# Kernel optimization log

Hardware: AMD Instinct MI355X
Metric: run time of the kernel (lower is better)

## Reference

```python
import jax, jax.numpy as jnp
import numpy as np

# PEPS grid configuration (matches init_kwargs)
X, Y = 4, 4            # xnodes, ynodes
D = 6                  # bond_dim
P = 2                  # features_in (physical dim)
F = 10                 # features_out (forced by result.view([10]))
CX, CY = X // 2, Y // 2  # center node carries the output leg
BATCH = 2048


def node_labels(i, j):
    # bond labels after the physical index is contracted away; axis order: up, left, down, right, out
    labs = []
    if i > 0: labs.append(f'v{i-1}_{j}')   # up bond (shared with row i-1)
    if j > 0: labs.append(f'h{i}_{j-1}')   # left bond (shared with col j-1)
    if i < X - 1: labs.append(f'v{i}_{j}') # down bond
    if j < Y - 1: labs.append(f'h{i}_{j}') # right bond
    if (i, j) == (CX, CY): labs.append('o')  # output leg on center node
    return labs


def node_shape(i, j):
    shp = [P]  # physical axis first (input_nodes[i][j][0] ^ peps_nodes[i][j][0])
    shp += [D] * (int(i > 0) + int(j > 0) + int(i < X - 1) + int(j < Y - 1))
    if (i, j) == (CX, CY): shp.append(F)
    return tuple(shp)


def setup_inputs() -> dict:
    key = jax.random.key(0)
    keys = jax.random.split(key, X * Y + 1)
    inp = {"x": jax.random.normal(keys[0], (BATCH, X, Y, P), dtype=jnp.float32)}
    k = 1
    for i in range(X):
        for j in range(Y):
            # simple_peps uniform init with std=0.01
            inp[f"w{i}{j}"] = jax.random.uniform(keys[k], node_shape(i, j), dtype=jnp.float32, minval=-0.01, maxval=0.01)
            k += 1
    return inp


def _td(a, alabs, b, blabs):
    """Label-tracked tensordot over all shared bond labels."""
    shared = [l for l in alabs if l in blabs]
    ai = [alabs.index(l) for l in shared]
    bi = [blabs.index(l) for l in shared]
    out = jnp.tensordot(a, b, axes=(ai, bi))
    labs = [l for l in alabs if l not in shared] + [l for l in blabs if l not in shared]
    return out, labs


def _contract_sample(xs, ws):
    # xs: [X, Y, P] one sample; ws: list-of-lists of node tensors
    # 1) contract each input vector into its PEPS node over the physical axis,
    #    then L2-normalize each contracted node (as in func())
    nodes = []
    for i in range(X):
        row = []
        for j in range(Y):
            t = jnp.tensordot(xs[i, j], ws[i][j], axes=(0, 0))
            t = t / jnp.linalg.norm(t)
            row.append(t)
        nodes.append(row)
    # 2) exact contraction of the 2D network, row-by-row boundary sweep
    cur, labs = nodes[0][0], node_labels(0, 0)
    for j in range(1, Y):
        cur, labs = _td(cur, labs, nodes[0][j], node_labels(0, j))
    for i in range(1, X):
        for j in range(Y):
            cur, labs = _td(cur, labs, nodes[i][j], node_labels(i, j))
    out = cur.reshape(F)  # result.view([10])
    return out / jnp.linalg.norm(out)


def reference(x, w00, w01, w02, w03, w10, w11, w12, w13,
              w20, w21, w22, w23, w30, w31, w32, w33):
    ws = [[w00, w01, w02, w03],
          [w10, w11, w12, w13],
          [w20, w21, w22, w23],
          [w30, w31, w32, w33]]
    return jax.vmap(lambda s: _contract_sample(s, ws))(x)  # [B, F]
```

## Files before the change

### kernel.cpp

```cpp
#include <hip/hip_runtime.h>
#include <math.h>

#define NT 128
#define NS 64

struct PW { const float* w[16]; int perp[16]; };

#define TLT 64
#define TRT 20800
#define BLT 41536
#define RTT 62272

template<int X1, int X2, int Y1, int Y2, int U, int L,
         int AX1, int AX2, int AU, int AL,
         int BU, int BLs, int BY1, int BY2,
         int OX1, int OX2, int OY1, int OY2>
__device__ __forceinline__ void contract(const float* __restrict__ A,
                                         const float* __restrict__ Bm,
                                         float* __restrict__ O, int tid) {
    constexpr int ROWS = X1 * X2 * Y1;
    for (int r = tid; r < ROWS; r += NT) {
        const int x1 = r / (X2 * Y1);
        const int rm = r - x1 * (X2 * Y1);
        const int x2 = rm / Y1;
        const int y1 = rm - x2 * Y1;
        const float* __restrict__ Ab = A + x1 * AX1 + x2 * AX2;
        const float* __restrict__ Bb = Bm + y1 * BY1;
        float acc[Y2];
#pragma unroll
        for (int t = 0; t < Y2; t++) acc[t] = 0.f;
#pragma unroll
        for (int u = 0; u < U; u++) {
#pragma unroll
            for (int l = 0; l < L; l++) {
                const float a = Ab[u * AU + l * AL];
                const float* __restrict__ Bp = Bb + u * BU + l * BLs;
#pragma unroll
                for (int t = 0; t < Y2; t++) acc[t] += a * Bp[t * BY2];
            }
        }
        float* __restrict__ Ob = O + x1 * OX1 + x2 * OX2 + y1 * OY1;
#pragma unroll
        for (int t = 0; t < Y2; t++) Ob[t * OY2] = acc[t];
    }
}

template<int M, int DST>
__device__ __forceinline__ void csel(float* __restrict__ L, const float* __restrict__ W, int tid) {
    for (int e = tid; e < M; e += NT) L[DST + e] = W[e];
}

__global__ __launch_bounds__(NT) void prep(PW pw, float* __restrict__ ws) {
    __shared__ float L[4356];
    constexpr int bA = 0, bB = 1296, bC = 2592, sA = 3888, sB = 4104, sC = 4320;
    const int tid = threadIdx.x, bid = blockIdx.x;
    if (bid < 16) {
        const int p = bid;
        csel<36, sC>(L, pw.w[0] + ((p >> 0) & 1) * 36, tid);
        csel<216, sA>(L, pw.w[1] + ((p >> 1) & 1) * 216, tid);
        __syncthreads();
        contract<1,6,6,6,6,1,  0,6,1,0,  36,0,6,1,  0,36,6,1>(L+sC, L+sA, L+sB, tid);
        csel<216, bA>(L, pw.w[4] + ((p >> 2) & 1) * 216, tid);
        __syncthreads();
        contract<1,36,6,6,6,1,  0,1,36,0,  36,0,6,1,  0,36,6,1>(L+sB, L+bA, L+bB, tid);
        csel<1296, bC>(L, pw.w[5] + ((p >> 3) & 1) * 1296, tid);
        __syncthreads();
        contract<6,6,6,6,6,6,  36,6,216,1,  216,36,6,1,  216*16,6*16,1*16,36*16>(L+bB, L+bC, ws + TLT + p, tid);
    } else if (bid < 32) {
        const int p = bid - 16;
        csel<216, sA>(L, pw.w[2] + ((p >> 0) & 1) * 216, tid);
        csel<36, sC>(L, pw.w[3] + ((p >> 1) & 1) * 36, tid);
        __syncthreads();
        contract<1,36,1,6,6,1,  0,6,1,0,  6,0,0,1,  0,6,0,1>(L+sA, L+sC, L+sB, tid);
        csel<216, bA>(L, pw.w[7] + ((p >> 2) & 1) * 216, tid);
        __syncthreads();
        contract<1,36,6,6,6,1,  0,6,1,0,  36,0,6,1,  0,36,6,1>(L+sB, L+bA, L+bB, tid);
        csel<1296, bC>(L, pw.w[6] + ((p >> 3) & 1) * 1296, tid);
        __syncthreads();
        contract<6,6,6,6,6,6,  36,6,216,1,  36,6,216,1,  36*16,6*16,216*16,1*16>(L+bC, L+bB, ws + TRT + p, tid);
    } else if (bid < 48) {
        const int p = bid - 32;
        csel<36, sC>(L, pw.w[12] + ((p >> 0) & 1) * 36, tid);
        csel<216, sA>(L, pw.w[8] + ((p >> 1) & 1) * 216, tid);
        __syncthreads();
        contract<1,6,6,6,6,1,  0,1,6,0,  6,0,36,1,  0,36,6,1>(L+sC, L+sA, L+sB, tid);
        csel<216, bA>(L, pw.w[13] + ((p >> 2) & 1) * 216, tid);
        __syncthreads();
        contract<1,36,6,6,6,1,  0,1,36,0,  6,0,36,1,  0,36,6,1>(L+sB, L+bA, L+bB, tid);
        csel<1296, bC>(L, pw.w[9] + ((p >> 3) & 1) * 1296, tid);
        __syncthreads();
        contract<6,6,6,6,6,6,  216,1,36,6,  36,6,216,1,  216*16,1*16,36*16,6*16>(L+bB, L+bC, ws + BLT + p, tid);
    } else if (bid < 56) {
        const int p = bid - 48;
        csel<216, sA>(L, pw.w[11] + ((p >> 0) & 1) * 216, tid);
        csel<36, sC>(L, pw.w[15] + ((p >> 1) & 1) * 36, tid);
        __syncthreads();
        contract<6,6,1,6,6,1,  36,6,1,0,  6,0,0,1,  36,6,0,1>(L+sA, L+sC, L+sB, tid);
        csel<216, bA>(L, pw.w[14] + ((p >> 2) & 1) * 216, tid);
        __syncthreads();
        contract<6,6,6,6,6,1,  36,6,1,0,  1,0,36,6,  216*8,1*8,6*8,36*8>(L+sB, L+bA, ws + RTT + p, tid);
    } else {
        const int n = bid - 56;
        const float* __restrict__ W = pw.w[n];
        const int m = pw.perp[n];
        float s00 = 0.f, s01 = 0.f, s11 = 0.f;
        for (int e = tid; e < m; e += NT) {
            float a = W[e], b = W[m + e];
            s00 += a * a; s01 += a * b; s11 += b * b;
        }
        for (int off = 32; off > 0; off >>= 1) {
            s00 += __shfl_down(s00, off, 64);
            s01 += __shfl_down(s01, off, 64);
            s11 += __shfl_down(s11, off, 64);
        }
        const int lane = tid & 63, wv = tid >> 6;
        if (lane == 0) { L[wv * 3 + 0] = s00; L[wv * 3 + 1] = s01; L[wv * 3 + 2] = s11; }
        __syncthreads();
        if (tid == 0) {
            ws[n * 3 + 0] = L[0] + L[3];
            ws[n * 3 + 1] = L[1] + L[4];
            ws[n * 3 + 2] = L[2] + L[5];
        }
    }
}


template<int PC, int GOFF>
__device__ __forceinline__ void sweep1(float* __restrict__ dst, const float* __restrict__ tab,
                                       const float* __restrict__ gam, int tid) {
    float g[PC];
#pragma unroll
    for (int c = 0; c < PC; c++) g[c] = gam[GOFF + c];
    for (int e = tid; e < 1296; e += NS) {
        const float4* __restrict__ tp = (const float4*)(tab + e * PC);
        float a = 0.f;
#pragma unroll
        for (int c = 0; c < PC / 4; c++) {
            const float4 v = tp[c];
            a += v.x * g[4*c] + v.y * g[4*c+1] + v.z * g[4*c+2] + v.w * g[4*c+3];
        }
        dst[e] = a;
    }
}

template<int SXH, int SXL, int SYH, int SYL>
__device__ __forceinline__ void kmm1(const float* __restrict__ A, const float* __restrict__ B,
                                     float* __restrict__ O, int tid) {
    if (tid < 54) {
        const int xg = tid / 3, yg = tid - xg * 3;
        const int x0 = xg * 2, y0 = yg * 12;
        float acc0[12], acc1[12];
#pragma unroll
        for (int j = 0; j < 12; j++) { acc0[j] = 0.f; acc1[j] = 0.f; }
#pragma unroll
        for (int k = 0; k < 36; k++) {
            const float2 a = *(const float2*)(A + k * 36 + x0);
            const float* __restrict__ Bp = B + k * 36 + y0;
            const float4 v0 = *(const float4*)(Bp);
            const float4 v1 = *(const float4*)(Bp + 4);
            const float4 v2 = *(const float4*)(Bp + 8);
            const float bv[12] = {v0.x,v0.y,v0.z,v0.w, v1.x,v1.y,v1.z,v1.w, v2.x,v2.y,v2.z,v2.w};
#pragma unroll
            for (int j = 0; j < 12; j++) {
                acc0[j] += a.x * bv[j];
                acc1[j] += a.y * bv[j];
            }
        }
#pragma unroll
        for (int i = 0; i < 2; i++) {
            const int xx = x0 + i;
            const int xh = xx / 6, xl = xx - xh * 6;
#pragma unroll
            for (int j = 0; j < 12; j++) {
                const int yy = y0 + j;
                const int yh = yy / 6, yl = yy - yh * 6;
                O[xh * SXH + xl * SXL + yh * SYH + yl * SYL] = (i == 0) ? acc0[j] : acc1[j];
            }
        }
    }
}

__global__ __launch_bounds__(NS) void peps_main(const float* __restrict__ x, PW pw,
                                                const float* __restrict__ ws,
                                                float* __restrict__ out) {
    __shared__ float A[1296], B[1296], C[1296];
    __shared__ float cfa[16], cfb[16], gam[56];

    const int tid = threadIdx.x;
    const int s = blockIdx.x;
    const float* __restrict__ gram = ws;

    if (tid < 16) {
        const float a = x[s * 32 + tid * 2 + 0];
        const float b = x[s * 32 + tid * 2 + 1];
        const float g0 = gram[tid*3+0], g1 = gram[tid*3+1], g2 = gram[tid*3+2];
        const float inv = 1.f / sqrtf(a*a*g0 + 2.f*a*b*g1 + b*b*g2);
        cfa[tid] = a * inv; cfb[tid] = b * inv;
    }
    __syncthreads();

    if (tid < 56) {
        const int u = tid;
        int p, nl0, nl1, nl2, nl3, nb;
        if (u < 16)      { p = u;      nl0 = 0;  nl1 = 1;  nl2 = 4;  nl3 = 5; nb = 4; }
        else if (u < 32) { p = u - 16; nl0 = 2;  nl1 = 3;  nl2 = 7;  nl3 = 6; nb = 4; }
        else if (u < 48) { p = u - 32; nl0 = 12; nl1 = 8;  nl2 = 13; nl3 = 9; nb = 4; }
        else             { p = u - 48; nl0 = 11; nl1 = 15; nl2 = 14; nl3 = 0; nb = 3; }
        float gv = ((p >> 0) & 1) ? cfb[nl0] : cfa[nl0];
        gv      *= ((p >> 1) & 1) ? cfb[nl1] : cfa[nl1];
        gv      *= ((p >> 2) & 1) ? cfb[nl2] : cfa[nl2];
        if (nb == 4) gv *= ((p >> 3) & 1) ? cfb[nl3] : cfa[nl3];
        gam[u] = gv;
    }
    __syncthreads();

    sweep1<16, 0>(A, ws + TLT, gam, tid);
    sweep1<16, 16>(B, ws + TRT, gam, tid);
    __syncthreads();
    kmm1<216, 36, 6, 1>(A, B, C, tid);
    __syncthreads();
    sweep1<16, 32>(A, ws + BLT, gam, tid);
    __syncthreads();
    kmm1<6, 216, 1, 36>(C, A, B, tid);
    __syncthreads();
    sweep1<8, 48>(C, ws + RTT, gam, tid);
    __syncthreads();
    kmm1<216, 36, 6, 1>(B, C, A, tid);
    __syncthreads();

    {
        const float al = cfa[10], be = cfb[10];
        const float* __restrict__ w0 = pw.w[10];
        const float* __restrict__ w1 = w0 + 12960;
        float p[10];
#pragma unroll
        for (int o = 0; o < 10; o++) p[o] = 0.f;
        for (int e = tid; e < 1296; e += NS) {
            const float Ev = A[e];
            const float* __restrict__ q0 = w0 + e * 10;
            const float* __restrict__ q1 = w1 + e * 10;
#pragma unroll
            for (int o = 0; o < 10; o++) p[o] += Ev * (al * q0[o] + be * q1[o]);
        }
#pragma unroll
        for (int o = 0; o < 10; o++)
            for (int off = 32; off > 0; off >>= 1)
                p[o] += __shfl_down(p[o], off, 64);
        if (tid == 0) {
            float ss = 0.f;
#pragma unroll
            for (int o = 0; o < 10; o++) ss += p[o] * p[o];
            const float inv = 1.f / sqrtf(ss);
#pragma unroll
            for (int o = 0; o < 10; o++) out[s * 10 + o] = p[o] * inv;
        }
    }
}

extern "C" void kernel_launch(void* const* d_in, const int* in_sizes, int n_in,
                              void* d_out, int out_size, void* d_ws, size_t ws_size,
                              hipStream_t stream) {
    PW pw;
    for (int k = 0; k < 16; k++) {
        pw.w[k] = (const float*)d_in[1 + k];
        pw.perp[k] = in_sizes[1 + k] / 2;
    }
    float* ws = (float*)d_ws;
    prep<<<72, NT, 0, stream>>>(pw, ws);

    const float* x = (const float*)d_in[0];
    const int B = out_size / 10;
    peps_main<<<B, NS, 0, stream>>>(x, pw, ws, (float*)d_out);
}
```

Before: 164.9 us.

## Process two samples per block to share weight-table loads

Each block now contracts two batch samples at once. The sweep tables, the kmm inner loops and the final center-node weights are loaded once and applied to both samples, which halves global table traffic per sample and doubles the independent FMA work per thread. In exchange the block uses about 31KB of LDS instead of about 16KB, kmm needs more registers, and the grid is half as large. It assumes an even batch size.

New measurement: 158.7 us. 1.04x faster.

```diff
diff --git a/kernel.cpp b/kernel.cpp
--- a/kernel.cpp
+++ b/kernel.cpp
@@ -126,44 +126,57 @@
 
 
 template<int PC, int GOFF>
-__device__ __forceinline__ void sweep1(float* __restrict__ dst, const float* __restrict__ tab,
+__device__ __forceinline__ void sweep2(float* __restrict__ dst0, float* __restrict__ dst1,
+                                       const float* __restrict__ tab,
                                        const float* __restrict__ gam, int tid) {
-    float g[PC];
-#pragma unroll
-    for (int c = 0; c < PC; c++) g[c] = gam[GOFF + c];
+    float g0[PC], g1[PC];
+#pragma unroll
+    for (int c = 0; c < PC; c++) { g0[c] = gam[GOFF + c]; g1[c] = gam[56 + GOFF + c]; }
     for (int e = tid; e < 1296; e += NS) {
         const float4* __restrict__ tp = (const float4*)(tab + e * PC);
-        float a = 0.f;
+        float a0 = 0.f, a1 = 0.f;
 #pragma unroll
         for (int c = 0; c < PC / 4; c++) {
             const float4 v = tp[c];
-            a += v.x * g[4*c] + v.y * g[4*c+1] + v.z * g[4*c+2] + v.w * g[4*c+3];
-        }
-        dst[e] = a;
+            a0 += v.x * g0[4*c] + v.y * g0[4*c+1] + v.z * g0[4*c+2] + v.w * g0[4*c+3];
+            a1 += v.x * g1[4*c] + v.y * g1[4*c+1] + v.z * g1[4*c+2] + v.w * g1[4*c+3];
+        }
+        dst0[e] = a0;
+        dst1[e] = a1;
     }
 }
 
 template<int SXH, int SXL, int SYH, int SYL>
-__device__ __forceinline__ void kmm1(const float* __restrict__ A, const float* __restrict__ B,
-                                     float* __restrict__ O, int tid) {
+__device__ __forceinline__ void kmm2(const float* __restrict__ A0, const float* __restrict__ B0,
+                                     float* __restrict__ O0,
+                                     const float* __restrict__ A1, const float* __restrict__ B1,
+                                     float* __restrict__ O1, int tid) {
     if (tid < 54) {
         const int xg = tid / 3, yg = tid - xg * 3;
         const int x0 = xg * 2, y0 = yg * 12;
-        float acc0[12], acc1[12];
-#pragma unroll
-        for (int j = 0; j < 12; j++) { acc0[j] = 0.f; acc1[j] = 0.f; }
+        float p00[12], p01[12], p10[12], p11[12];
+#pragma unroll
+        for (int j = 0; j < 12; j++) { p00[j] = 0.f; p01[j] = 0.f; p10[j] = 0.f; p11[j] = 0.f; }
 #pragma unroll
         for (int k = 0; k < 36; k++) {
-            const float2 a = *(const float2*)(A + k * 36 + x0);
-            const float* __restrict__ Bp = B + k * 36 + y0;
-            const float4 v0 = *(const float4*)(Bp);
-            const float4 v1 = *(const float4*)(Bp + 4);
-            const float4 v2 = *(const float4*)(Bp + 8);
-            const float bv[12] = {v0.x,v0.y,v0.z,v0.w, v1.x,v1.y,v1.z,v1.w, v2.x,v2.y,v2.z,v2.w};
+            const float2 a0 = *(const float2*)(A0 + k * 36 + x0);
+            const float2 a1 = *(const float2*)(A1 + k * 36 + x0);
+            const float* __restrict__ Bp0 = B0 + k * 36 + y0;
+            const float* __restrict__ Bp1 = B1 + k * 36 + y0;
+            const float4 u0 = *(const float4*)(Bp0);
+            const float4 u1 = *(const float4*)(Bp0 + 4);
+            const float4 u2 = *(const float4*)(Bp0 + 8);
+            const float4 w0 = *(const float4*)(Bp1);
+            const float4 w1 = *(const float4*)(Bp1 + 4);
+            const float4 w2 = *(const float4*)(Bp1 + 8);
+            const float bv0[12] = {u0.x,u0.y,u0.z,u0.w, u1.x,u1.y,u1.z,u1.w, u2.x,u2.y,u2.z,u2.w};
+            const float bv1[12] = {w0.x,w0.y,w0.z,w0.w, w1.x,w1.y,w1.z,w1.w, w2.x,w2.y,w2.z,w2.w};
 #pragma unroll
             for (int j = 0; j < 12; j++) {
-                acc0[j] += a.x * bv[j];
-                acc1[j] += a.y * bv[j];
+                p00[j] += a0.x * bv0[j];
+                p01[j] += a0.y * bv0[j];
+                p10[j] += a1.x * bv1[j];
+                p11[j] += a1.y * bv1[j];
             }
         }
 #pragma unroll
@@ -174,7 +187,9 @@
             for (int j = 0; j < 12; j++) {
                 const int yy = y0 + j;
                 const int yh = yy / 6, yl = yy - yh * 6;
-                O[xh * SXH + xl * SXL + yh * SYH + yl * SYL] = (i == 0) ? acc0[j] : acc1[j];
+                const int off = xh * SXH + xl * SXL + yh * SYH + yl * SYL;
+                O0[off] = (i == 0) ? p00[j] : p01[j];
+                O1[off] = (i == 0) ? p10[j] : p11[j];
             }
         }
     }
@@ -183,76 +198,91 @@
 __global__ __launch_bounds__(NS) void peps_main(const float* __restrict__ x, PW pw,
                                                 const float* __restrict__ ws,
                                                 float* __restrict__ out) {
-    __shared__ float A[1296], B[1296], C[1296];
-    __shared__ float cfa[16], cfb[16], gam[56];
+    __shared__ float lds[7776];
+    __shared__ float cfa[2][16], cfb[2][16], gam[112];
+    float* const A0 = lds;          float* const B0 = lds + 1296; float* const C0 = lds + 2592;
+    float* const A1 = lds + 3888;   float* const B1 = lds + 5184; float* const C1 = lds + 6480;
 
     const int tid = threadIdx.x;
-    const int s = blockIdx.x;
+    const int s0 = blockIdx.x * 2;
     const float* __restrict__ gram = ws;
 
-    if (tid < 16) {
-        const float a = x[s * 32 + tid * 2 + 0];
-        const float b = x[s * 32 + tid * 2 + 1];
-        const float g0 = gram[tid*3+0], g1 = gram[tid*3+1], g2 = gram[tid*3+2];
+    if (tid < 32) {
+        const int sl = tid >> 4, n = tid & 15;
+        const float a = x[(s0 + sl) * 32 + n * 2 + 0];
+        const float b = x[(s0 + sl) * 32 + n * 2 + 1];
+        const float g0 = gram[n*3+0], g1 = gram[n*3+1], g2 = gram[n*3+2];
         const float inv = 1.f / sqrtf(a*a*g0 + 2.f*a*b*g1 + b*b*g2);
-        cfa[tid] = a * inv; cfb[tid] = b * inv;
-    }
-    __syncthreads();
-
-    if (tid < 56) {
-        const int u = tid;
+        cfa[sl][n] = a * inv; cfb[sl][n] = b * inv;
+    }
+    __syncthreads();
+
+    for (int t = tid; t < 112; t += NS) {
+        const int sl = t / 56, u = t - sl * 56;
         int p, nl0, nl1, nl2, nl3, nb;
         if (u < 16)      { p = u;      nl0 = 0;  nl1 = 1;  nl2 = 4;  nl3 = 5; nb = 4; }
         else if (u < 32) { p = u - 16; nl0 = 2;  nl1 = 3;  nl2 = 7;  nl3 = 6; nb = 4; }
         else if (u < 48) { p = u - 32; nl0 = 12; nl1 = 8;  nl2 = 13; nl3 = 9; nb = 4; }
         else             { p = u - 48; nl0 = 11; nl1 = 15; nl2 = 14; nl3 = 0; nb = 3; }
-        float gv = ((p >> 0) & 1) ? cfb[nl0] : cfa[nl0];
-        gv      *= ((p >> 1) & 1) ? cfb[nl1] : cfa[nl1];
-        gv      *= ((p >> 2) & 1) ? cfb[nl2] : cfa[nl2];
-        if (nb == 4) gv *= ((p >> 3) & 1) ? cfb[nl3] : cfa[nl3];
-        gam[u] = gv;
-    }
-    __syncthreads();
-
-    sweep1<16, 0>(A, ws + TLT, gam, tid);
-    sweep1<16, 16>(B, ws + TRT, gam, tid);
-    __syncthreads();
-    kmm1<216, 36, 6, 1>(A, B, C, tid);
-    __syncthreads();
-    sweep1<16, 32>(A, ws + BLT, gam, tid);
-    __syncthreads();
-    kmm1<6, 216, 1, 36>(C, A, B, tid);
-    __syncthreads();
-    sweep1<8, 48>(C, ws + RTT, gam, tid);
-    __syncthreads();
-    kmm1<216, 36, 6, 1>(B, C, A, tid);
+        float gv = ((p >> 0) & 1) ? cfb[sl][nl0] : cfa[sl][nl0];
+        gv      *= ((p >> 1) & 1) ? cfb[sl][nl1] : cfa[sl][nl1];
+        gv      *= ((p >> 2) & 1) ? cfb[sl][nl2] : cfa[sl][nl2];
+        if (nb == 4) gv *= ((p >> 3) & 1) ? cfb[sl][nl3] : cfa[sl][nl3];
+        gam[t] = gv;
+    }
+    __syncthreads();
+
+    sweep2<16, 0>(A0, A1, ws + TLT, gam, tid);
+    sweep2<16, 16>(B0, B1, ws + TRT, gam, tid);
+    __syncthreads();
+    kmm2<216, 36, 6, 1>(A0, B0, C0, A1, B1, C1, tid);
+    __syncthreads();
+    sweep2<16, 32>(A0, A1, ws + BLT, gam, tid);
+    __syncthreads();
+    kmm2<6, 216, 1, 36>(C0, A0, B0, C1, A1, B1, tid);
+    __syncthreads();
+    sweep2<8, 48>(C0, C1, ws + RTT, gam, tid);
+    __syncthreads();
+    kmm2<216, 36, 6, 1>(B0, C0, A0, B1, C1, A1, tid);
     __syncthreads();
 
     {
-        const float al = cfa[10], be = cfb[10];
+        const float a0 = cfa[0][10], b0 = cfb[0][10];
+        const float a1 = cfa[1][10], b1 = cfb[1][10];
         const float* __restrict__ w0 = pw.w[10];
         const float* __restrict__ w1 = w0 + 12960;
-        float p[10];
-#pragma unroll
-        for (int o = 0; o < 10; o++) p[o] = 0.f;
+        float p0[10], p1[10];
+#pragma unroll
+        for (int o = 0; o < 10; o++) { p0[o] = 0.f; p1[o] = 0.f; }
         for (int e = tid; e < 1296; e += NS) {
-            const float Ev = A[e];
+            const float E0 = A0[e];
+            const float E1 = A1[e];
             const float* __restrict__ q0 = w0 + e * 10;
             const float* __restrict__ q1 = w1 + e * 10;
 #pragma unroll
-            for (int o = 0; o < 10; o++) p[o] += Ev * (al * q0[o] + be * q1[o]);
+            for (int o = 0; o < 10; o++) {
+                const float v0 = q0[o], v1 = q1[o];
+                p0[o] += E0 * (a0 * v0 + b0 * v1);
+                p1[o] += E1 * (a1 * v0 + b1 * v1);
+            }
         }
 #pragma unroll
         for (int o = 0; o < 10; o++)
-            for (int off = 32; off > 0; off >>= 1)
-                p[o] += __shfl_down(p[o], off, 64);
+            for (int off = 32; off > 0; off >>= 1) {
+                p0[o] += __shfl_down(p0[o], off, 64);
+                p1[o] += __shfl_down(p1[o], off, 64);
+            }
         if (tid == 0) {
-            float ss = 0.f;
-#pragma unroll
-            for (int o = 0; o < 10; o++) ss += p[o] * p[o];
-            const float inv = 1.f / sqrtf(ss);
-#pragma unroll
-            for (int o = 0; o < 10; o++) out[s * 10 + o] = p[o] * inv;
+            float ss0 = 0.f, ss1 = 0.f;
+#pragma unroll
+            for (int o = 0; o < 10; o++) { ss0 += p0[o] * p0[o]; ss1 += p1[o] * p1[o]; }
+            const float i0 = 1.f / sqrtf(ss0);
+            const float i1 = 1.f / sqrtf(ss1);
+#pragma unroll
+            for (int o = 0; o < 10; o++) {
+                out[s0 * 10 + o] = p0[o] * i0;
+                out[(s0 + 1) * 10 + o] = p1[o] * i1;
+            }
         }
     }
 }
@@ -270,5 +300,5 @@
 
     const float* x = (const float*)d_in[0];
     const int B = out_size / 10;
-    peps_main<<<B, NS, 0, stream>>>(x, pw, ws, (float*)d_out);
-}
+    peps_main<<<B / 2, NS, 0, stream>>>(x, pw, ws, (float*)d_out);
+}
```
